# Kernel optimization log

Hardware: AMD Instinct MI355X
Metric: run time of the kernel (lower is better)

The kernel has to match this reference:

```python
import jax, jax.numpy as jnp
import numpy as np

B, T, D_IN, H, D_OUT = 4096, 512, 10, 20, 2


def setup_inputs() -> dict:
    key = jax.random.key(0)
    ks = jax.random.split(key, 12)
    s = 1.0 / np.sqrt(H)  # PyTorch-style uniform bound scale (use normal*s)
    return {
        "x": jax.random.normal(ks[0], (B, T, D_IN), jnp.float32),
        "w_ih0": jax.random.normal(ks[1], (H, D_IN), jnp.float32) * s,
        "w_hh0": jax.random.normal(ks[2], (H, H), jnp.float32) * s,
        "b_ih0": jax.random.normal(ks[3], (H,), jnp.float32) * s,
        "b_hh0": jax.random.normal(ks[4], (H,), jnp.float32) * s,
        "w_ih1": jax.random.normal(ks[5], (H, H), jnp.float32) * s,
        "w_hh1": jax.random.normal(ks[6], (H, H), jnp.float32) * s,
        "b_ih1": jax.random.normal(ks[7], (H,), jnp.float32) * s,
        "b_hh1": jax.random.normal(ks[8], (H,), jnp.float32) * s,
        "fc_w": jax.random.normal(ks[9], (D_OUT, H), jnp.float32) * s,
        "fc_b": jax.random.normal(ks[10], (D_OUT,), jnp.float32) * s,
    }


def _rnn_layer(inp, w_ih, w_hh, b_ih, b_hh):
    # inp: [B, T, Din]. Precompute input projection once (batched GEMM),
    # then scan the sequential recurrence: h_t = tanh(x_t W_ih^T + b_ih + h_{t-1} W_hh^T + b_hh)
    xp = jnp.einsum('btd,hd->bth', inp, w_ih) + (b_ih + b_hh)  # [B, T, H]

    def step(h, xt):
        h = jnp.tanh(xt + h @ w_hh.T)
        return h, h

    h0 = jnp.zeros((inp.shape[0], w_hh.shape[0]), inp.dtype)
    _, hs = jax.lax.scan(step, h0, jnp.swapaxes(xp, 0, 1))  # hs: [T, B, H]
    return jnp.swapaxes(hs, 0, 1)  # [B, T, H]


def reference(x, w_ih0, w_hh0, b_ih0, b_hh0, w_ih1, w_hh1, b_ih1, b_hh1, fc_w, fc_b):
    h1 = _rnn_layer(x, w_ih0, w_hh0, b_ih0, b_hh0)
    h2 = _rnn_layer(h1, w_ih1, w_hh1, b_ih1, b_hh1)
    last = h2[:, -1, :]  # [B, H]
    return last @ fc_w.T + fc_b  # [B, D_OUT]
```

## Files before the change

### kernel.cpp

```cpp
#include <hip/hip_runtime.h>
#include <cstdint>

constexpr int B_   = 4096;
constexpr int T_   = 512;
constexpr int DIN  = 10;
constexpr int H_   = 20;
constexpr int DOUT = 2;

constexpr int SPW = 3;
constexpr int CH  = 2;
constexpr int XV  = CH * DIN / 4;

#define CFENCE() asm volatile("" ::: "memory")

__device__ __forceinline__ float fast_tanh(float v) {
    float e = __builtin_amdgcn_exp2f(v * 2.885390082f );
    float r = __builtin_amdgcn_rcpf(e + 1.0f);
    return fmaf(-2.0f, r, 1.0f);
}

extern "C" __global__ void __launch_bounds__(64, 2)
rnn_fused(const float* __restrict__ x,
          const float* __restrict__ w_ih0, const float* __restrict__ w_hh0,
          const float* __restrict__ b_ih0, const float* __restrict__ b_hh0,
          const float* __restrict__ w_ih1, const float* __restrict__ w_hh1,
          const float* __restrict__ b_ih1, const float* __restrict__ b_hh1,
          const float* __restrict__ fc_w, const float* __restrict__ fc_b,
          float* __restrict__ out)
{
    const int lane = threadIdx.x;
    const int sl   = lane / H_;
    const int i    = lane - sl * H_;
    const int samp = blockIdx.x * SPW + sl;
    const int sc   = (samp < B_) ? samp : (B_ - 1);
    const int slc  = (sl < SPW) ? sl : SPW;

    __shared__ __align__(16) float h1s[SPW + 1][H_];
    __shared__ __align__(16) float h2s[SPW + 1][H_];

    float wi0[DIN];
    {
        const float2* p = reinterpret_cast<const float2*>(w_ih0 + i * DIN);
        #pragma unroll
        for (int k = 0; k < DIN / 2; ++k) {
            float2 v = p[k];
            wi0[2 * k] = v.x; wi0[2 * k + 1] = v.y;
        }
    }
    float wh0[H_], wi1[H_], wh1[H_];
    {
        const float4* p0 = reinterpret_cast<const float4*>(w_hh0 + i * H_);
        const float4* p1 = reinterpret_cast<const float4*>(w_ih1 + i * H_);
        const float4* p2 = reinterpret_cast<const float4*>(w_hh1 + i * H_);
        #pragma unroll
        for (int k = 0; k < H_ / 4; ++k) {
            float4 a = p0[k]; wh0[4*k]=a.x; wh0[4*k+1]=a.y; wh0[4*k+2]=a.z; wh0[4*k+3]=a.w;
            float4 b = p1[k]; wi1[4*k]=b.x; wi1[4*k+1]=b.y; wi1[4*k+2]=b.z; wi1[4*k+3]=b.w;
            float4 c = p2[k]; wh1[4*k]=c.x; wh1[4*k+1]=c.y; wh1[4*k+2]=c.z; wh1[4*k+3]=c.w;
        }
    }
    const float bias0 = b_ih0[i] + b_hh0[i];
    const float bias1 = b_ih1[i] + b_hh1[i];

    float h1[H_], h2[H_];
    #pragma unroll
    for (int j = 0; j < H_; ++j) { h1[j] = 0.0f; h2[j] = 0.0f; }

    const float4* xb = reinterpret_cast<const float4*>(x + (size_t)sc * (T_ * DIN));

    float4 xv[XV];
    #pragma unroll
    for (int k = 0; k < XV; ++k) xv[k] = xb[k];

    for (int t0 = 0; t0 < T_; t0 += CH) {
        float xp[CH];
        #pragma unroll
        for (int m = 0; m < CH; ++m) xp[m] = bias0;
        #pragma unroll
        for (int k = 0; k < XV; ++k) {
            int idx = 4 * k;
            xp[(idx+0)/DIN] = fmaf(xv[k].x, wi0[(idx+0)%DIN], xp[(idx+0)/DIN]);
            xp[(idx+1)/DIN] = fmaf(xv[k].y, wi0[(idx+1)%DIN], xp[(idx+1)/DIN]);
            xp[(idx+2)/DIN] = fmaf(xv[k].z, wi0[(idx+2)%DIN], xp[(idx+2)/DIN]);
            xp[(idx+3)/DIN] = fmaf(xv[k].w, wi0[(idx+3)%DIN], xp[(idx+3)/DIN]);
        }

        {
            const int t0n = (t0 + CH < T_) ? (t0 + CH) : 0;
            #pragma unroll
            for (int k = 0; k < XV; ++k) xv[k] = xb[(t0n * DIN) / 4 + k];
        }

        #pragma unroll
        for (int m = 0; m < CH; ++m) {
            float a0 = xp[m], a1 = 0.f, a2 = 0.f, a3 = 0.f;
            #pragma unroll
            for (int j = 0; j < H_; j += 4) {
                a0 = fmaf(h1[j+0], wh0[j+0], a0);
                a1 = fmaf(h1[j+1], wh0[j+1], a1);
                a2 = fmaf(h1[j+2], wh0[j+2], a2);
                a3 = fmaf(h1[j+3], wh0[j+3], a3);
            }
            float h1n = fast_tanh((a0 + a1) + (a2 + a3));

            CFENCE();
            h1s[slc][i] = h1n;
            CFENCE();

            float b0 = bias1, b1 = 0.f, b2 = 0.f, b3 = 0.f;
            #pragma unroll
            for (int j = 0; j < H_; j += 4) {
                b0 = fmaf(h2[j+0], wh1[j+0], b0);
                b1 = fmaf(h2[j+1], wh1[j+1], b1);
                b2 = fmaf(h2[j+2], wh1[j+2], b2);
                b3 = fmaf(h2[j+3], wh1[j+3], b3);
            }

            #pragma unroll
            for (int k = 0; k < H_ / 4; ++k) {
                float4 v = reinterpret_cast<const float4*>(&h1s[slc][0])[k];
                h1[4*k]=v.x; h1[4*k+1]=v.y; h1[4*k+2]=v.z; h1[4*k+3]=v.w;
            }
            CFENCE();

            #pragma unroll
            for (int j = 0; j < H_; j += 4) {
                b0 = fmaf(h1[j+0], wi1[j+0], b0);
                b1 = fmaf(h1[j+1], wi1[j+1], b1);
                b2 = fmaf(h1[j+2], wi1[j+2], b2);
                b3 = fmaf(h1[j+3], wi1[j+3], b3);
            }
            float h2n = fast_tanh((b0 + b1) + (b2 + b3));

            CFENCE();
            h2s[slc][i] = h2n;
            CFENCE();
            #pragma unroll
            for (int k = 0; k < H_ / 4; ++k) {
                float4 v = reinterpret_cast<const float4*>(&h2s[slc][0])[k];
                h2[4*k]=v.x; h2[4*k+1]=v.y; h2[4*k+2]=v.z; h2[4*k+3]=v.w;
            }
            CFENCE();
        }
    }

    if (sl < SPW && samp < B_ && i < DOUT) {
        float acc = fc_b[i];
        #pragma unroll
        for (int j = 0; j < H_; ++j) acc = fmaf(h2[j], fc_w[i * H_ + j], acc);
        out[samp * DOUT + i] = acc;
    }
}

extern "C" void kernel_launch(void* const* d_in, const int* in_sizes, int n_in,
                              void* d_out, int out_size, void* d_ws, size_t ws_size,
                              hipStream_t stream) {
    (void)in_sizes; (void)n_in; (void)d_ws; (void)ws_size; (void)out_size;
    const float* x     = (const float*)d_in[0];
    const float* w_ih0 = (const float*)d_in[1];
    const float* w_hh0 = (const float*)d_in[2];
    const float* b_ih0 = (const float*)d_in[3];
    const float* b_hh0 = (const float*)d_in[4];
    const float* w_ih1 = (const float*)d_in[5];
    const float* w_hh1 = (const float*)d_in[6];
    const float* b_ih1 = (const float*)d_in[7];
    const float* b_hh1 = (const float*)d_in[8];
    const float* fc_w  = (const float*)d_in[9];
    const float* fc_b  = (const float*)d_in[10];
    float* out = (float*)d_out;

    const int grid = (B_ + SPW - 1) / SPW;
    hipLaunchKernelGGL(rnn_fused, dim3(grid), dim3(64), 0, stream,
                       x, w_ih0, w_hh0, b_ih0, b_hh0,
                       w_ih1, w_hh1, b_ih1, b_hh1, fc_w, fc_b, out);
}
```

Measured before the change: 167.9 us.

## Rewrite RNN kernel as 4-lane-per-sample fp16 dot2 with DPP exchange and layer skew

Replaces the 20-lanes-per-sample layout with 4 lanes per sample (16 samples per wave), each lane owning 5 hidden units. Weights are pre-scaled by the tanh exp2 constant and packed to fp16 for v_dot2 accumulation into fp32, and hidden state is exchanged across the quad with DPP moves instead of LDS. The two layers are skewed by one step so a single fused step computes layer-1 at t and layer-2 at t-1 from the same state vector. This cuts lane waste and shuffle latency on the serial recurrence, but fp16 weights and state lower accuracy over 512 steps.

```diff
diff --git a/kernel.cpp b/kernel.cpp
--- a/kernel.cpp
+++ b/kernel.cpp
@@ -7,148 +7,203 @@
 constexpr int H_   = 20;
 constexpr int DOUT = 2;
 
-constexpr int SPW = 3;
-constexpr int CH  = 2;
-constexpr int XV  = CH * DIN / 4;
+typedef float    v2f  __attribute__((ext_vector_type(2)));
+typedef _Float16 h2t  __attribute__((ext_vector_type(2)));
+typedef __fp16   fp2t __attribute__((ext_vector_type(2)));
+
+constexpr float SCL = 2.885390082f;
 
 #define CFENCE() asm volatile("" ::: "memory")
 
-__device__ __forceinline__ float fast_tanh(float v) {
-    float e = __builtin_amdgcn_exp2f(v * 2.885390082f );
+__device__ __forceinline__ float fdot2(h2t a, h2t b, float c) {
+#if __has_builtin(__builtin_amdgcn_fdot2)
+    return __builtin_amdgcn_fdot2(a, b, c, false);
+#else
+    return fmaf((float)a.x, (float)b.x, fmaf((float)a.y, (float)b.y, c));
+#endif
+}
+
+__device__ __forceinline__ float tanh_pre(float s) {
+    float e = __builtin_amdgcn_exp2f(s);
     float r = __builtin_amdgcn_rcpf(e + 1.0f);
     return fmaf(-2.0f, r, 1.0f);
 }
 
-extern "C" __global__ void __launch_bounds__(64, 2)
-rnn_fused(const float* __restrict__ x,
-          const float* __restrict__ w_ih0, const float* __restrict__ w_hh0,
-          const float* __restrict__ b_ih0, const float* __restrict__ b_hh0,
-          const float* __restrict__ w_ih1, const float* __restrict__ w_hh1,
-          const float* __restrict__ b_ih1, const float* __restrict__ b_hh1,
-          const float* __restrict__ fc_w, const float* __restrict__ fc_b,
-          float* __restrict__ out)
+union HI { int i; h2t h; fp2t f; };
+
+#define QP1 0x39
+#define QP2 0x4E
+#define QP3 0x93
+
+extern "C" __global__ void __launch_bounds__(64)
+__attribute__((amdgpu_waves_per_eu(1, 1)))
+rnn_quad(const float* __restrict__ x,
+         const float* __restrict__ w_ih0, const float* __restrict__ w_hh0,
+         const float* __restrict__ b_ih0, const float* __restrict__ b_hh0,
+         const float* __restrict__ w_ih1, const float* __restrict__ w_hh1,
+         const float* __restrict__ b_ih1, const float* __restrict__ b_hh1,
+         const float* __restrict__ fc_w, const float* __restrict__ fc_b,
+         float* __restrict__ out)
 {
     const int lane = threadIdx.x;
-    const int sl   = lane / H_;
-    const int i    = lane - sl * H_;
-    const int samp = blockIdx.x * SPW + sl;
-    const int sc   = (samp < B_) ? samp : (B_ - 1);
-    const int slc  = (sl < SPW) ? sl : SPW;
-
-    __shared__ __align__(16) float h1s[SPW + 1][H_];
-    __shared__ __align__(16) float h2s[SPW + 1][H_];
-
-    float wi0[DIN];
-    {
-        const float2* p = reinterpret_cast<const float2*>(w_ih0 + i * DIN);
-        #pragma unroll
-        for (int k = 0; k < DIN / 2; ++k) {
-            float2 v = p[k];
-            wi0[2 * k] = v.x; wi0[2 * k + 1] = v.y;
-        }
-    }
-    float wh0[H_], wi1[H_], wh1[H_];
-    {
-        const float4* p0 = reinterpret_cast<const float4*>(w_hh0 + i * H_);
-        const float4* p1 = reinterpret_cast<const float4*>(w_ih1 + i * H_);
-        const float4* p2 = reinterpret_cast<const float4*>(w_hh1 + i * H_);
-        #pragma unroll
-        for (int k = 0; k < H_ / 4; ++k) {
-            float4 a = p0[k]; wh0[4*k]=a.x; wh0[4*k+1]=a.y; wh0[4*k+2]=a.z; wh0[4*k+3]=a.w;
-            float4 b = p1[k]; wi1[4*k]=b.x; wi1[4*k+1]=b.y; wi1[4*k+2]=b.z; wi1[4*k+3]=b.w;
-            float4 c = p2[k]; wh1[4*k]=c.x; wh1[4*k+1]=c.y; wh1[4*k+2]=c.z; wh1[4*k+3]=c.w;
-        }
-    }
-    const float bias0 = b_ih0[i] + b_hh0[i];
-    const float bias1 = b_ih1[i] + b_hh1[i];
-
-    float h1[H_], h2[H_];
-    #pragma unroll
-    for (int j = 0; j < H_; ++j) { h1[j] = 0.0f; h2[j] = 0.0f; }
-
-    const float4* xb = reinterpret_cast<const float4*>(x + (size_t)sc * (T_ * DIN));
-
-    float4 xv[XV];
-    #pragma unroll
-    for (int k = 0; k < XV; ++k) xv[k] = xb[k];
-
-    for (int t0 = 0; t0 < T_; t0 += CH) {
-        float xp[CH];
-        #pragma unroll
-        for (int m = 0; m < CH; ++m) xp[m] = bias0;
-        #pragma unroll
-        for (int k = 0; k < XV; ++k) {
-            int idx = 4 * k;
-            xp[(idx+0)/DIN] = fmaf(xv[k].x, wi0[(idx+0)%DIN], xp[(idx+0)/DIN]);
-            xp[(idx+1)/DIN] = fmaf(xv[k].y, wi0[(idx+1)%DIN], xp[(idx+1)/DIN]);
-            xp[(idx+2)/DIN] = fmaf(xv[k].z, wi0[(idx+2)%DIN], xp[(idx+2)/DIN]);
-            xp[(idx+3)/DIN] = fmaf(xv[k].w, wi0[(idx+3)%DIN], xp[(idx+3)/DIN]);
-        }
-
-        {
-            const int t0n = (t0 + CH < T_) ? (t0 + CH) : 0;
+    const int q    = lane >> 2;
+    const int c    = lane & 3;
+    const int samp = blockIdx.x * 16 + q;
+
+    __shared__ float ldsF[16][20];
+
+    int cid[4];
+    cid[0] = c;
+    cid[1] = __builtin_amdgcn_mov_dpp(c, QP1, 0xF, 0xF, true);
+    cid[2] = __builtin_amdgcn_mov_dpp(c, QP2, 0xF, 0xF, true);
+    cid[3] = __builtin_amdgcn_mov_dpp(c, QP3, 0xF, 0xF, true);
+
+    h2t W0[5][12];
+    h2t W1[5][20];
+    h2t WX[5][5];
+    float bx[5], b1v[5];
+    #pragma unroll
+    for (int r = 0; r < 5; ++r) {
+        const int rho = 5 * c + r;
+        #pragma unroll
+        for (int g = 0; g < 4; ++g) {
+            const int bse = 5 * cid[g];
+            const float* u0 = w_hh0 + rho * H_ + bse;
+            const float* ui = w_ih1 + rho * H_ + bse;
+            const float* uh = w_hh1 + rho * H_ + bse;
+            W0[r][g*3+0] = h2t{(_Float16)(SCL*u0[0]), (_Float16)(SCL*u0[1])};
+            W0[r][g*3+1] = h2t{(_Float16)(SCL*u0[2]), (_Float16)(SCL*u0[3])};
+            W0[r][g*3+2] = h2t{(_Float16)(SCL*u0[4]), (_Float16)0.f};
+            W1[r][g*5+0] = h2t{(_Float16)(SCL*ui[0]), (_Float16)(SCL*ui[1])};
+            W1[r][g*5+1] = h2t{(_Float16)(SCL*ui[2]), (_Float16)(SCL*ui[3])};
+            W1[r][g*5+2] = h2t{(_Float16)(SCL*ui[4]), (_Float16)(SCL*uh[0])};
+            W1[r][g*5+3] = h2t{(_Float16)(SCL*uh[1]), (_Float16)(SCL*uh[2])};
+            W1[r][g*5+4] = h2t{(_Float16)(SCL*uh[3]), (_Float16)(SCL*uh[4])};
+        }
+        #pragma unroll
+        for (int k = 0; k < 5; ++k)
+            WX[r][k] = h2t{(_Float16)(SCL * w_ih0[rho * DIN + 2*k]),
+                           (_Float16)(SCL * w_ih0[rho * DIN + 2*k + 1])};
+        bx[r]  = SCL * (b_ih0[rho] + b_hh0[rho]);
+        b1v[r] = SCL * (b_ih1[rho] + b_hh1[rho]);
+    }
+
+    h2t S[4][5];
+    #pragma unroll
+    for (int g = 0; g < 4; ++g)
+        #pragma unroll
+        for (int k = 0; k < 5; ++k) S[g][k] = h2t{(_Float16)0.f, (_Float16)0.f};
+
+    const float* xr = x + (size_t)samp * (T_ * DIN);
+
+    v2f xraw[5];
+    float xp[5];
+    auto load_raw = [&](int t) {
+        const v2f* p = reinterpret_cast<const v2f*>(xr + (size_t)t * DIN);
+        #pragma unroll
+        for (int k = 0; k < 5; ++k) xraw[k] = p[k];
+    };
+    auto make_xp = [&]() {
+        HI xd[5];
+        #pragma unroll
+        for (int k = 0; k < 5; ++k)
+            xd[k].f = __builtin_amdgcn_cvt_pkrtz(xraw[k].x, xraw[k].y);
+        #pragma unroll
+        for (int r = 0; r < 5; ++r) {
+            float p0 = bx[r], p1 = 0.f;
+            p0 = fdot2(xd[0].h, WX[r][0], p0);
+            p1 = fdot2(xd[1].h, WX[r][1], p1);
+            p0 = fdot2(xd[2].h, WX[r][2], p0);
+            p1 = fdot2(xd[3].h, WX[r][3], p1);
+            p0 = fdot2(xd[4].h, WX[r][4], p0);
+            xp[r] = p0 + p1;
+        }
+    };
+
+    auto full_step = [&](float keep) {
+        float h1n[5], h2n[5];
+        #pragma unroll
+        for (int r = 0; r < 5; ++r) {
+            float a0 = xp[r], a1 = 0.f;
             #pragma unroll
-            for (int k = 0; k < XV; ++k) xv[k] = xb[(t0n * DIN) / 4 + k];
-        }
-
-        #pragma unroll
-        for (int m = 0; m < CH; ++m) {
-            float a0 = xp[m], a1 = 0.f, a2 = 0.f, a3 = 0.f;
+            for (int g = 0; g < 4; ++g) {
+                a0 = fdot2(S[g][0], W0[r][g*3+0], a0);
+                a1 = fdot2(S[g][1], W0[r][g*3+1], a1);
+                a0 = fdot2(S[g][2], W0[r][g*3+2], a0);
+            }
+            h1n[r] = tanh_pre(a0 + a1);
+            float q0 = b1v[r], q1 = 0.f, q2 = 0.f, q3 = 0.f;
             #pragma unroll
-            for (int j = 0; j < H_; j += 4) {
-                a0 = fmaf(h1[j+0], wh0[j+0], a0);
-                a1 = fmaf(h1[j+1], wh0[j+1], a1);
-                a2 = fmaf(h1[j+2], wh0[j+2], a2);
-                a3 = fmaf(h1[j+3], wh0[j+3], a3);
+            for (int g = 0; g < 4; ++g) {
+                q0 = fdot2(S[g][0], W1[r][g*5+0], q0);
+                q1 = fdot2(S[g][1], W1[r][g*5+1], q1);
+                q2 = fdot2(S[g][2], W1[r][g*5+2], q2);
+                q3 = fdot2(S[g][3], W1[r][g*5+3], q3);
+                q0 = fdot2(S[g][4], W1[r][g*5+4], q0);
             }
-            float h1n = fast_tanh((a0 + a1) + (a2 + a3));
-
-            CFENCE();
-            h1s[slc][i] = h1n;
-            CFENCE();
-
-            float b0 = bias1, b1 = 0.f, b2 = 0.f, b3 = 0.f;
-            #pragma unroll
-            for (int j = 0; j < H_; j += 4) {
-                b0 = fmaf(h2[j+0], wh1[j+0], b0);
-                b1 = fmaf(h2[j+1], wh1[j+1], b1);
-                b2 = fmaf(h2[j+2], wh1[j+2], b2);
-                b3 = fmaf(h2[j+3], wh1[j+3], b3);
-            }
-
-            #pragma unroll
-            for (int k = 0; k < H_ / 4; ++k) {
-                float4 v = reinterpret_cast<const float4*>(&h1s[slc][0])[k];
-                h1[4*k]=v.x; h1[4*k+1]=v.y; h1[4*k+2]=v.z; h1[4*k+3]=v.w;
-            }
-            CFENCE();
-
-            #pragma unroll
-            for (int j = 0; j < H_; j += 4) {
-                b0 = fmaf(h1[j+0], wi1[j+0], b0);
-                b1 = fmaf(h1[j+1], wi1[j+1], b1);
-                b2 = fmaf(h1[j+2], wi1[j+2], b2);
-                b3 = fmaf(h1[j+3], wi1[j+3], b3);
-            }
-            float h2n = fast_tanh((b0 + b1) + (b2 + b3));
-
-            CFENCE();
-            h2s[slc][i] = h2n;
-            CFENCE();
-            #pragma unroll
-            for (int k = 0; k < H_ / 4; ++k) {
-                float4 v = reinterpret_cast<const float4*>(&h2s[slc][0])[k];
-                h2[4*k]=v.x; h2[4*k+1]=v.y; h2[4*k+2]=v.z; h2[4*k+3]=v.w;
-            }
-            CFENCE();
-        }
-    }
-
-    if (sl < SPW && samp < B_ && i < DOUT) {
-        float acc = fc_b[i];
-        #pragma unroll
-        for (int j = 0; j < H_; ++j) acc = fmaf(h2[j], fc_w[i * H_ + j], acc);
-        out[samp * DOUT + i] = acc;
+            h2n[r] = keep * tanh_pre((q0 + q1) + (q2 + q3));
+        }
+        HI d0, d1, d2, d3, d4;
+        d0.f = __builtin_amdgcn_cvt_pkrtz(h1n[0], h1n[1]);
+        d1.f = __builtin_amdgcn_cvt_pkrtz(h1n[2], h1n[3]);
+        d2.f = __builtin_amdgcn_cvt_pkrtz(h1n[4], h2n[0]);
+        d3.f = __builtin_amdgcn_cvt_pkrtz(h2n[1], h2n[2]);
+        d4.f = __builtin_amdgcn_cvt_pkrtz(h2n[3], h2n[4]);
+        S[0][0] = d0.h; S[0][1] = d1.h; S[0][2] = d2.h; S[0][3] = d3.h; S[0][4] = d4.h;
+#define GSLOT(G, CTRL)                                                          \
+        { HI t0_, t1_, t2_, t3_, t4_;                                           \
+          t0_.i = __builtin_amdgcn_mov_dpp(d0.i, CTRL, 0xF, 0xF, true);         \
+          t1_.i = __builtin_amdgcn_mov_dpp(d1.i, CTRL, 0xF, 0xF, true);         \
+          t2_.i = __builtin_amdgcn_mov_dpp(d2.i, CTRL, 0xF, 0xF, true);         \
+          t3_.i = __builtin_amdgcn_mov_dpp(d3.i, CTRL, 0xF, 0xF, true);         \
+          t4_.i = __builtin_amdgcn_mov_dpp(d4.i, CTRL, 0xF, 0xF, true);         \
+          S[G][0] = t0_.h; S[G][1] = t1_.h; S[G][2] = t2_.h;                    \
+          S[G][3] = t3_.h; S[G][4] = t4_.h; }
+        GSLOT(1, QP1)
+        GSLOT(2, QP2)
+        GSLOT(3, QP3)
+#undef GSLOT
+    };
+
+    load_raw(0);
+    make_xp();
+    load_raw(1);
+
+    full_step(0.0f);
+    make_xp();
+    load_raw(2);
+
+    for (int t = 1; t <= 510; ++t) {
+        full_step(1.0f);
+        make_xp();
+        load_raw((t + 2 <= 511) ? (t + 2) : 511);
+    }
+    full_step(1.0f);
+
+    float h2f[5];
+    #pragma unroll
+    for (int r = 0; r < 5; ++r) {
+        float q0 = b1v[r], q1 = 0.f, q2 = 0.f, q3 = 0.f;
+        #pragma unroll
+        for (int g = 0; g < 4; ++g) {
+            q0 = fdot2(S[g][0], W1[r][g*5+0], q0);
+            q1 = fdot2(S[g][1], W1[r][g*5+1], q1);
+            q2 = fdot2(S[g][2], W1[r][g*5+2], q2);
+            q3 = fdot2(S[g][3], W1[r][g*5+3], q3);
+            q0 = fdot2(S[g][4], W1[r][g*5+4], q0);
+        }
+        h2f[r] = tanh_pre((q0 + q1) + (q2 + q3));
+    }
+    CFENCE();
+    #pragma unroll
+    for (int r = 0; r < 5; ++r) ldsF[q][5 * c + r] = h2f[r];
+    CFENCE();
+
+    if (c < DOUT) {
+        float acc = fc_b[c];
+        #pragma unroll
+        for (int j = 0; j < H_; ++j) acc = fmaf(ldsF[q][j], fc_w[c * H_ + j], acc);
+        out[samp * DOUT + c] = acc;
     }
 }
 
@@ -169,8 +224,7 @@
     const float* fc_b  = (const float*)d_in[10];
     float* out = (float*)d_out;
 
-    const int grid = (B_ + SPW - 1) / SPW;
-    hipLaunchKernelGGL(rnn_fused, dim3(grid), dim3(64), 0, stream,
+    hipLaunchKernelGGL(rnn_quad, dim3(B_ / 16), dim3(64), 0, stream,
                        x, w_ih0, w_hh0, b_ih0, b_hh0,
                        w_ih1, w_hh1, b_ih1, b_hh1, fc_w, fc_b, out);
 }
```

After: 318.8 us. 1.9x slower.
